# Optimization experiments

Measured on AMD Instinct MI355X. Metric: run time of the kernel, lower is better.

Reference implementation:

```python
import jax, jax.numpy as jnp
import numpy as np

N = 50000      # nodes
E = 800000     # edges (avg degree 16)
IN = 128       # input feature dim
D = 128        # embed dim (heads=1, concat)
SLOPE = 0.2    # GATv2Conv default negative_slope


def setup_inputs() -> dict:
    key = jax.random.key(0)
    ks = jax.random.split(key, 16)
    s_in = 1.0 / np.sqrt(IN)
    s_d = 1.0 / np.sqrt(D)
    inp = {
        "node_fts": jax.random.normal(ks[0], (N, IN), dtype=jnp.float32),
        "edge_index": jax.random.randint(ks[1], (2, E), 0, N, dtype=jnp.int64),
        # layer 1 (in_dim -> embed_dim)
        "Wl1": jax.random.normal(ks[2], (IN, D), dtype=jnp.float32) * s_in,
        "bl1": jnp.zeros((D,), dtype=jnp.float32),
        "Wr1": jax.random.normal(ks[3], (IN, D), dtype=jnp.float32) * s_in,
        "br1": jnp.zeros((D,), dtype=jnp.float32),
        "att1": jax.random.normal(ks[4], (D,), dtype=jnp.float32) * s_d,
        "bias1": jnp.zeros((D,), dtype=jnp.float32),
        # layer 2 (embed_dim -> embed_dim)
        "Wl2": jax.random.normal(ks[5], (D, D), dtype=jnp.float32) * s_d,
        "bl2": jnp.zeros((D,), dtype=jnp.float32),
        "Wr2": jax.random.normal(ks[6], (D, D), dtype=jnp.float32) * s_d,
        "br2": jnp.zeros((D,), dtype=jnp.float32),
        "att2": jax.random.normal(ks[7], (D,), dtype=jnp.float32) * s_d,
        "bias2": jnp.zeros((D,), dtype=jnp.float32),
    }
    return inp


def gatv2_layer(x, src, dst, Wl, bl, Wr, br, att, bias):
    # GATv2Conv (heads=1, share_weights=False):
    #   x_j (source message features) = lin_l(x), x_i (target) = lin_r(x)
    xl = x @ Wl + bl                                      # [N, D]
    xr = x @ Wr + br                                      # [N, D]
    e = jax.nn.leaky_relu(xl[src] + xr[dst], SLOPE)       # [E, D]
    logits = e @ att                                      # [E]
    # softmax over incoming edges of each target node
    m = jax.ops.segment_max(logits, dst, num_segments=N)  # [N], -inf for isolated
    m = jnp.where(jnp.isneginf(m), 0.0, m)
    a = jnp.exp(logits - m[dst])                          # [E]
    s = jax.ops.segment_sum(a, dst, num_segments=N)       # [N]
    a = a / jnp.maximum(s[dst], 1e-16)
    out = jax.ops.segment_sum(a[:, None] * xl[src], dst, num_segments=N)  # [N, D]
    return out + bias


def reference(node_fts, edge_index,
              Wl1, bl1, Wr1, br1, att1, bias1,
              Wl2, bl2, Wr2, br2, att2, bias2):
    src, dst = edge_index[0], edge_index[1]
    x = jax.nn.relu(gatv2_layer(node_fts, src, dst, Wl1, bl1, Wr1, br1, att1, bias1))
    x = jax.nn.relu(gatv2_layer(x, src, dst, Wl2, bl2, Wr2, br2, att2, bias2))
    return x
```

## Files before the change

kernel.cpp:

```cpp
#include <hip/hip_runtime.h>
#include <hip/hip_bf16.h>
#include <hip/hip_fp16.h>

#define N_NODES 50000
#define N_EDGES 800000
#define DIM 128
#define NGROUPS (N_NODES / 16)
#define LROW2 132
#define KBUCKET 196
#define BCAP 5120
#define EPB 2000

typedef __attribute__((ext_vector_type(8))) _Float16 hfrag8;
typedef __attribute__((ext_vector_type(4))) float f32x4;
typedef _Float16 h2 __attribute__((ext_vector_type(2)));

__device__ __forceinline__ h2 u2h(uint u){ union{uint u; h2 h;} c; c.u = u; return c.h; }


__global__ __launch_bounds__(256) void bucket_scatter_k(
    const int* __restrict__ src, const int* __restrict__ dst,
    int* __restrict__ bucket_cnt, uint* __restrict__ bucketdata)
{
  __shared__ int cnt[KBUCKET], base[KBUCKET], cur[KBUCKET];
  int tid = threadIdx.x;
  for (int t = tid; t < KBUCKET; t += 256) { cnt[t] = 0; cur[t] = 0; }
  __syncthreads();
  int e0 = blockIdx.x * EPB;
  int dreg[8];
  #pragma unroll
  for (int it = 0; it < 8; it++) {
    int i = it*256 + tid;
    dreg[it] = (i < EPB) ? dst[e0 + i] : -1;
    if (i < EPB) atomicAdd(&cnt[dreg[it] >> 8], 1);
  }
  __syncthreads();
  for (int t = tid; t < KBUCKET; t += 256)
    base[t] = atomicAdd(&bucket_cnt[t], cnt[t]);
  __syncthreads();
  #pragma unroll
  for (int it = 0; it < 8; it++) {
    int i = it*256 + tid;
    if (i < EPB) {
      int s = src[e0 + i], d = dreg[it];
      int b = d >> 8;
      int r = atomicAdd(&cur[b], 1);
      bucketdata[(size_t)b * BCAP + base[b] + r] = ((uint)s << 8) | (uint)(d & 255);
    }
  }
}

__global__ __launch_bounds__(64) void prep_w(
    const float* __restrict__ Wl1, const float* __restrict__ Wr1,
    const float* __restrict__ Wl2, const float* __restrict__ Wr2,
    _Float16* __restrict__ wb, int* __restrict__ bucket_cnt)
{
  int bid = blockIdx.x;
  if (bid == 0) {
    for (int t = threadIdx.x; t < KBUCKET; t += 64) bucket_cnt[t] = 0;
  }
  int layer = bid >> 6, rest = bid & 63;
  int C = rest >> 4, g = rest & 15;
  int lane = threadIdx.x;
  int m = lane & 15, q = lane >> 4;
  int dim = g*16 + m;
  const float* W = layer ? (dim < 128 ? Wl2 : Wr2) : (dim < 128 ? Wl1 : Wr1);
  int dcol = dim & 127;
  _Float16 h[8];
  #pragma unroll
  for (int j = 0; j < 8; j++) {
    int k = C*32 + q*8 + j;
    h[j] = (_Float16)W[(size_t)k*DIM + dcol];
  }
  size_t off = ((size_t)bid*64 + lane)*8;
  *(hfrag8*)(wb + off) = *(hfrag8*)h;
}

__global__ __launch_bounds__(256) void gemm1_csr_k(
    const float* __restrict__ x, const _Float16* __restrict__ wb,
    const float* __restrict__ bl, const float* __restrict__ br,
    __half* __restrict__ xlh, __half* __restrict__ xrh,
    const int* __restrict__ bucket_cnt, const uint* __restrict__ bucketdata,
    int* __restrict__ row_start, int* __restrict__ csr_src)
{
  __shared__ float lds[4][16*LROW2];
  __shared__ int hist[256], cur[256];
  __shared__ int wsumA[4], wsumB[4];
  int tid = threadIdx.x;

  if (blockIdx.x < KBUCKET) {
    int b = blockIdx.x;
    int lane = tid & 63, w = tid >> 6;
    int vv = (tid < b) ? bucket_cnt[tid] : 0;
    #pragma unroll
    for (int off = 32; off > 0; off >>= 1) vv += __shfl_xor(vv, off, 64);
    if (lane == 0) wsumA[w] = vv;
    hist[tid] = 0;
    __syncthreads();
    int base_csr = wsumA[0] + wsumA[1] + wsumA[2] + wsumA[3];
    int cnt = bucket_cnt[b];
    int node0 = b << 8;
    const uint* bd = bucketdata + (size_t)b * BCAP;
    for (int i = tid; i < cnt; i += 256)
      atomicAdd(&hist[bd[i] & 255], 1);
    __syncthreads();
    int v = hist[tid];
    int inc = v;
    #pragma unroll
    for (int off = 1; off < 64; off <<= 1) {
      int y = __shfl_up(inc, off, 64);
      if (lane >= off) inc += y;
    }
    if (lane == 63) wsumB[w] = inc;
    __syncthreads();
    int wpre = 0;
    #pragma unroll
    for (int i = 0; i < 4; i++) if (i < w) wpre += wsumB[i];
    int excl = wpre + inc - v;
    int node = node0 + tid;
    if (node < N_NODES) row_start[node] = base_csr + excl;
    if (b == 0 && tid == 0) row_start[N_NODES] = N_EDGES;
    cur[tid] = excl;
    __syncthreads();
    for (int i = tid; i < cnt; i += 256) {
      uint p = bd[i];
      int r = atomicAdd(&cur[p & 255], 1);
      csr_src[base_csr + r] = (int)(p >> 8);
    }
    return;
  }

  int wv = tid >> 6, lane = tid & 63;
  int G = (blockIdx.x - KBUCKET) * 4 + wv;
  if (G >= NGROUPS) return;

  int m = lane & 15, q = lane >> 4;
  const float* xrow = x + (size_t)(G*16 + m)*DIM + q*8;

  f32x4 acc[16];
  #pragma unroll
  for (int g = 0; g < 16; g++) acc[g] = (f32x4)(0.f);

  #pragma unroll 1
  for (int C = 0; C < 4; C++) {
    float v[8];
    *(float4*)(v)     = *(const float4*)(xrow + C*32);
    *(float4*)(v + 4) = *(const float4*)(xrow + C*32 + 4);
    _Float16 hh[8];
    #pragma unroll
    for (int j = 0; j < 8; j++) hh[j] = (_Float16)v[j];
    hfrag8 ah = *(hfrag8*)hh;
    #pragma unroll
    for (int g = 0; g < 16; g++) {
      size_t boff = ((size_t)(C*16 + g)*64 + lane)*8;
      hfrag8 bh = *(const hfrag8*)(wb + boff);
      acc[g] = __builtin_amdgcn_mfma_f32_16x16x32_f16(ah, bh, acc[g], 0, 0, 0);
    }
  }

  float* wlds = lds[wv];
  int dcol = (lane & 31) * 4;
  int rowsel = lane >> 5;
  #pragma unroll
  for (int half = 0; half < 2; half++) {
    #pragma unroll
    for (int g = 0; g < 8; g++) {
      #pragma unroll
      for (int r = 0; r < 4; r++)
        wlds[(q*4 + r)*LROW2 + g*16 + m] = acc[half*8 + g][r];
    }
    const float* B = half ? br : bl;
    ushort* outh = half ? (ushort*)xrh : (ushort*)xlh;
    float4 bv = *(const float4*)(B + dcol);
    #pragma unroll
    for (int it = 0; it < 8; it++) {
      int i = it*2 + rowsel;
      float4 vv = *(const float4*)(wlds + i*LROW2 + dcol);
      int node = G*16 + i;
      __half2 h0 = __floats2half2_rn(vv.x + bv.x, vv.y + bv.y);
      __half2 h1 = __floats2half2_rn(vv.z + bv.z, vv.w + bv.w);
      uint2 pk = make_uint2(*(uint*)&h0, *(uint*)&h1);
      *(uint2*)(outh + (size_t)node*DIM + dcol) = pk;
    }
  }
}

__device__ __forceinline__ void gather_core(
    int node, int hl,
    const __half* __restrict__ xlh, const __half* __restrict__ xrh,
    const int* __restrict__ row_start, const int* __restrict__ csr_src,
    const float* __restrict__ att, const float* __restrict__ bias,
    float4& o0, float4& o1)
{
  int r0 = row_start[node];
  int deg = row_start[node + 1] - r0;
  int last = r0 + deg - 1;

  uint4 rx = *(const uint4*)((const ushort*)xrh + (size_t)node*DIM + hl*8);
  h2 xr01 = u2h(rx.x), xr23 = u2h(rx.y), xr45 = u2h(rx.z), xr67 = u2h(rx.w);
  const float* ap = att + hl*8;
  float4 af0 = *(const float4*)(ap);
  float4 af1 = *(const float4*)(ap + 4);
  h2 a01 = {(_Float16)af0.x, (_Float16)af0.y};
  h2 a23 = {(_Float16)af0.z, (_Float16)af0.w};
  h2 a45 = {(_Float16)af1.x, (_Float16)af1.y};
  h2 a67 = {(_Float16)af1.z, (_Float16)af1.w};
  const h2 c02 = {(_Float16)0.2f, (_Float16)0.2f};

  float l = 0.f;
  float b0a=0,b1a=0,b2a=0,b3a=0,b4a=0,b5a=0,b6a=0,b7a=0;
  const ushort* xbase = (const ushort*)xlh + hl*8;

  for (int t = 0; t < deg; t += 8) {
    int idx[8];
    #pragma unroll
    for (int j = 0; j < 8; j++) {
      int rr = r0 + t + j;
      idx[j] = csr_src[rr <= last ? rr : last];
    }
    uint4 raw[8];
    #pragma unroll
    for (int j = 0; j < 8; j++)
      raw[j] = *(const uint4*)(xbase + (size_t)idx[j]*DIM);
    #pragma unroll
    for (int j = 0; j < 8; j++) {
      h2 v01 = u2h(raw[j].x), v23 = u2h(raw[j].y);
      h2 v45 = u2h(raw[j].z), v67 = u2h(raw[j].w);
      h2 s01 = v01 + xr01, s23 = v23 + xr23;
      h2 s45 = v45 + xr45, s67 = v67 + xr67;
      s01 = __builtin_elementwise_max(s01, s01 * c02);
      s23 = __builtin_elementwise_max(s23, s23 * c02);
      s45 = __builtin_elementwise_max(s45, s45 * c02);
      s67 = __builtin_elementwise_max(s67, s67 * c02);
      float p = __builtin_amdgcn_fdot2(s01, a01, 0.f, false);
      p = __builtin_amdgcn_fdot2(s23, a23, p, false);
      p = __builtin_amdgcn_fdot2(s45, a45, p, false);
      p = __builtin_amdgcn_fdot2(s67, a67, p, false);
      #pragma unroll
      for (int o = 1; o <= 8; o <<= 1) p += __shfl_xor(p, o, 64);
      float w = (t + j < deg) ? __expf(p) : 0.f;
      l += w;
      b0a = fmaf(w, (float)v01.x, b0a); b1a = fmaf(w, (float)v01.y, b1a);
      b2a = fmaf(w, (float)v23.x, b2a); b3a = fmaf(w, (float)v23.y, b3a);
      b4a = fmaf(w, (float)v45.x, b4a); b5a = fmaf(w, (float)v45.y, b5a);
      b6a = fmaf(w, (float)v67.x, b6a); b7a = fmaf(w, (float)v67.y, b7a);
    }
  }

  float inv = 1.f / fmaxf(l, 1e-16f);
  const float* bp = bias + hl*8;
  float4 c0 = *(const float4*)(bp);
  float4 c1 = *(const float4*)(bp + 4);
  o0.x = fmaxf(fmaf(b0a, inv, c0.x), 0.f);
  o0.y = fmaxf(fmaf(b1a, inv, c0.y), 0.f);
  o0.z = fmaxf(fmaf(b2a, inv, c0.z), 0.f);
  o0.w = fmaxf(fmaf(b3a, inv, c0.w), 0.f);
  o1.x = fmaxf(fmaf(b4a, inv, c1.x), 0.f);
  o1.y = fmaxf(fmaf(b5a, inv, c1.y), 0.f);
  o1.z = fmaxf(fmaf(b6a, inv, c1.z), 0.f);
  o1.w = fmaxf(fmaf(b7a, inv, c1.w), 0.f);
}

__global__ __launch_bounds__(256) void fused_g1_gemm2_k(
    const __half* __restrict__ xlh, const __half* __restrict__ xrh,
    const int* __restrict__ row_start, const int* __restrict__ csr_src,
    const float* __restrict__ att, const float* __restrict__ bias,
    const _Float16* __restrict__ wb2,
    const float* __restrict__ bl2, const float* __restrict__ br2,
    __half* __restrict__ xlh2, __half* __restrict__ xrh2)
{
  __shared__ ushort xs[16*128];
  __shared__ ushort outs[16*256];
  int tid = threadIdx.x;
  int wv = tid >> 6, lane = tid & 63;
  int q4 = lane >> 4, hl = lane & 15;
  int nl = wv*4 + q4;
  int base = blockIdx.x * 16;

  float4 o0, o1;
  gather_core(base + nl, hl, xlh, xrh, row_start, csr_src, att, bias, o0, o1);
  __half2 p0 = __floats2half2_rn(o0.x, o0.y);
  __half2 p1 = __floats2half2_rn(o0.z, o0.w);
  __half2 p2 = __floats2half2_rn(o1.x, o1.y);
  __half2 p3 = __floats2half2_rn(o1.z, o1.w);
  uint4 pk = make_uint4(*(uint*)&p0, *(uint*)&p1, *(uint*)&p2, *(uint*)&p3);
  *(uint4*)((char*)xs + nl*256 + ((hl*16) ^ ((nl&7)<<4))) = pk;
  __syncthreads();

  int m = lane & 15, q = lane >> 4;
  f32x4 acc[4];
  #pragma unroll
  for (int g = 0; g < 4; g++) acc[g] = (f32x4)(0.f);
  #pragma unroll
  for (int C = 0; C < 4; C++) {
    hfrag8 ah = *(const hfrag8*)((const char*)xs + m*256 + ((C*64 + q*16) ^ ((m&7)<<4)));
    #pragma unroll
    for (int g = 0; g < 4; g++) {
      int gg = wv*4 + g;
      size_t boff = ((size_t)(C*16 + gg)*64 + lane)*8;
      hfrag8 bh = *(const hfrag8*)(wb2 + boff);
      acc[g] = __builtin_amdgcn_mfma_f32_16x16x32_f16(ah, bh, acc[g], 0, 0, 0);
    }
  }
  #pragma unroll
  for (int g = 0; g < 4; g++) {
    int gg = wv*4 + g;
    int dim = gg*16 + m;
    float bv = (gg < 8) ? bl2[dim] : br2[dim - 128];
    #pragma unroll
    for (int r = 0; r < 4; r++) {
      int row = q*4 + r;
      __half hv = __float2half_rn(acc[g][r] + bv);
      outs[row*256 + gg*16 + m] = *(ushort*)&hv;
    }
  }
  __syncthreads();
  #pragma unroll
  for (int p = 0; p < 2; p++) {
    int c = p*256 + tid;
    int row = c >> 5, off = c & 31;
    uint4 v = *(const uint4*)((const char*)outs + row*512 + off*16);
    int nodeo = base + row;
    int d0 = off*8;
    ushort* dstp = (d0 < 128) ? ((ushort*)xlh2 + (size_t)nodeo*DIM + d0)
                              : ((ushort*)xrh2 + (size_t)nodeo*DIM + (d0 - 128));
    *(uint4*)dstp = v;
  }
}

__global__ __launch_bounds__(256) void gat_gather2(
    const __half* __restrict__ xlh, const __half* __restrict__ xrh,
    const int* __restrict__ row_start, const int* __restrict__ csr_src,
    const float* __restrict__ att, const float* __restrict__ bias,
    float* __restrict__ outf)
{
  int wave = (blockIdx.x * 256 + threadIdx.x) >> 6;
  int lane = threadIdx.x & 63;
  int q4 = lane >> 4;
  int hl = lane & 15;
  int node = wave * 4 + q4;
  float4 o0, o1;
  gather_core(node, hl, xlh, xrh, row_start, csr_src, att, bias, o0, o1);
  float* op = outf + (size_t)node*DIM + hl*8;
  *(float4*)(op)     = o0;
  *(float4*)(op + 4) = o1;
}

extern "C" void kernel_launch(void* const* d_in, const int* in_sizes, int n_in,
                              void* d_out, int out_size, void* d_ws, size_t ws_size,
                              hipStream_t stream)
{
  const float* node_fts = (const float*)d_in[0];
  const int*  edge_index = (const int*)d_in[1];
  const float* Wl1 = (const float*)d_in[2];
  const float* bl1 = (const float*)d_in[3];
  const float* Wr1 = (const float*)d_in[4];
  const float* br1 = (const float*)d_in[5];
  const float* att1 = (const float*)d_in[6];
  const float* bias1 = (const float*)d_in[7];
  const float* Wl2 = (const float*)d_in[8];
  const float* bl2 = (const float*)d_in[9];
  const float* Wr2 = (const float*)d_in[10];
  const float* br2 = (const float*)d_in[11];
  const float* att2 = (const float*)d_in[12];
  const float* bias2 = (const float*)d_in[13];
  const int* src = edge_index;
  const int* dst = edge_index + N_EDGES;

  char* ws = (char*)d_ws;
  __half* xlh = (__half*)ws;               ws += (size_t)N_NODES*DIM*2;
  __half* xrh = (__half*)ws;               ws += (size_t)N_NODES*DIM*2;
  __half* xlh2 = (__half*)ws;              ws += (size_t)N_NODES*DIM*2;
  __half* xrh2 = (__half*)ws;              ws += (size_t)N_NODES*DIM*2;
  _Float16* wb = (_Float16*)ws;            ws += 2*4*16*64*8*2;
  int* row_start   = (int*)ws;             ws += (N_NODES+1)*4;
  int* csr_src     = (int*)ws;             ws += (size_t)N_EDGES*4;
  int* bucket_cnt  = (int*)ws;             ws += KBUCKET*4;
  uint* bucketdata = (uint*)ws;            ws += (size_t)KBUCKET*BCAP*4;

  const int W_LAYER = 4*16*64*8;

  int gemm_blocks = (NGROUPS + 3) / 4;
  int gather_blocks = N_NODES / 16;

  prep_w<<<128, 64, 0, stream>>>(Wl1, Wr1, Wl2, Wr2, wb, bucket_cnt);
  bucket_scatter_k<<<N_EDGES/EPB, 256, 0, stream>>>(src, dst, bucket_cnt, bucketdata);
  gemm1_csr_k<<<KBUCKET + gemm_blocks, 256, 0, stream>>>(
      node_fts, wb, bl1, br1, xlh, xrh,
      bucket_cnt, bucketdata, row_start, csr_src);
  fused_g1_gemm2_k<<<NGROUPS, 256, 0, stream>>>(
      xlh, xrh, row_start, csr_src, att1, bias1,
      wb + W_LAYER, bl2, br2, xlh2, xrh2);
  gat_gather2<<<gather_blocks, 256, 0, stream>>>(
      xlh2, xrh2, row_start, csr_src, att2, bias2, (float*)d_out);
}
```

Baseline: 218.1 us.

## Degree-sort nodes per bucket, pipeline gather loads, use DPP reductions

Builds a per-bucket permutation that groups nodes by in-degree so waves processing four nodes have balanced loop trip counts, and runs both gather kernels over permuted slots. Stores pre-scaled byte offsets in the CSR to avoid index multiplies, double-buffers neighbor row loads in 4-edge halves to overlap memory with compute, and replaces shuffle-xor reductions with DPP row operations. Adds indirection through perm and padding slots, and the DPP shift-based reduction may not broadcast the sum to all lanes.

Result: slower. 229.9 us (+5.4%).

```diff
diff --git a/kernel.cpp b/kernel.cpp
--- a/kernel.cpp
+++ b/kernel.cpp
@@ -10,12 +10,23 @@
 #define KBUCKET 196
 #define BCAP 5120
 #define EPB 2000
+#define NSLOT (KBUCKET*256)
 
 typedef __attribute__((ext_vector_type(8))) _Float16 hfrag8;
 typedef __attribute__((ext_vector_type(4))) float f32x4;
 typedef _Float16 h2 __attribute__((ext_vector_type(2)));
 
 __device__ __forceinline__ h2 u2h(uint u){ union{uint u; h2 h;} c; c.u = u; return c.h; }
+
+__device__ __forceinline__ float rowsum16(float p) {
+  union { float f; int i; } a, b;
+  a.f = p;
+  b.i = __builtin_amdgcn_update_dpp(0, a.i, 0x128, 0xF, 0xF, true); a.f += b.f;
+  b.i = __builtin_amdgcn_update_dpp(0, a.i, 0x124, 0xF, 0xF, true); a.f += b.f;
+  b.i = __builtin_amdgcn_update_dpp(0, a.i, 0x122, 0xF, 0xF, true); a.f += b.f;
+  b.i = __builtin_amdgcn_update_dpp(0, a.i, 0x121, 0xF, 0xF, true); a.f += b.f;
+  return a.f;
+}
 
 
 __global__ __launch_bounds__(256) void bucket_scatter_k(
@@ -81,11 +92,13 @@
     const float* __restrict__ bl, const float* __restrict__ br,
     __half* __restrict__ xlh, __half* __restrict__ xrh,
     const int* __restrict__ bucket_cnt, const uint* __restrict__ bucketdata,
-    int* __restrict__ row_start, int* __restrict__ csr_src)
+    int* __restrict__ row_start, int* __restrict__ csr_soff,
+    int* __restrict__ perm)
 {
   __shared__ float lds[4][16*LROW2];
   __shared__ int hist[256], cur[256];
   __shared__ int wsumA[4], wsumB[4];
+  __shared__ int dhist[64], dbase[64], dcur[64];
   int tid = threadIdx.x;
 
   if (blockIdx.x < KBUCKET) {
@@ -96,6 +109,7 @@
     for (int off = 32; off > 0; off >>= 1) vv += __shfl_xor(vv, off, 64);
     if (lane == 0) wsumA[w] = vv;
     hist[tid] = 0;
+    if (tid < 64) { dhist[tid] = 0; dcur[tid] = 0; }
     __syncthreads();
     int base_csr = wsumA[0] + wsumA[1] + wsumA[2] + wsumA[3];
     int cnt = bucket_cnt[b];
@@ -105,6 +119,9 @@
       atomicAdd(&hist[bd[i] & 255], 1);
     __syncthreads();
     int v = hist[tid];
+    int node = node0 + tid;
+    int degc = (node < N_NODES) ? min(v, 63) : 63;
+    atomicAdd(&dhist[degc], 1);
     int inc = v;
     #pragma unroll
     for (int off = 1; off < 64; off <<= 1) {
@@ -117,15 +134,26 @@
     #pragma unroll
     for (int i = 0; i < 4; i++) if (i < w) wpre += wsumB[i];
     int excl = wpre + inc - v;
-    int node = node0 + tid;
     if (node < N_NODES) row_start[node] = base_csr + excl;
     if (b == 0 && tid == 0) row_start[N_NODES] = N_EDGES;
     cur[tid] = excl;
+    if (tid < 64) {
+      int c = dhist[tid];
+      int ic = c;
+      #pragma unroll
+      for (int off = 1; off < 64; off <<= 1) {
+        int y = __shfl_up(ic, off, 64);
+        if (tid >= off) ic += y;
+      }
+      dbase[tid] = ic - c;
+    }
     __syncthreads();
+    int rank = dbase[degc] + atomicAdd(&dcur[degc], 1);
+    perm[node0 + rank] = node;
     for (int i = tid; i < cnt; i += 256) {
       uint p = bd[i];
       int r = atomicAdd(&cur[p & 255], 1);
-      csr_src[base_csr + r] = (int)(p >> 8);
+      csr_soff[base_csr + r] = (int)(p & 0xFFFFFF00u);
     }
     return;
   }
@@ -175,25 +203,63 @@
     #pragma unroll
     for (int it = 0; it < 8; it++) {
       int i = it*2 + rowsel;
-      float4 vv = *(const float4*)(wlds + i*LROW2 + dcol);
+      float4 vv2 = *(const float4*)(wlds + i*LROW2 + dcol);
       int node = G*16 + i;
-      __half2 h0 = __floats2half2_rn(vv.x + bv.x, vv.y + bv.y);
-      __half2 h1 = __floats2half2_rn(vv.z + bv.z, vv.w + bv.w);
+      __half2 h0 = __floats2half2_rn(vv2.x + bv.x, vv2.y + bv.y);
+      __half2 h1 = __floats2half2_rn(vv2.z + bv.z, vv2.w + bv.w);
       uint2 pk = make_uint2(*(uint*)&h0, *(uint*)&h1);
       *(uint2*)(outh + (size_t)node*DIM + dcol) = pk;
     }
   }
 }
 
+
+#define GAT_LDI(OFF, TBASE)                                             \
+  _Pragma("unroll")                                                     \
+  for (int j = 0; j < 4; j++) {                                         \
+    int rr = r0 + (TBASE) + j;                                          \
+    OFF[j] = csr_soff[rr <= last ? rr : last];                          \
+  }
+
+#define GAT_LDR(OFF, RAW)                                               \
+  _Pragma("unroll")                                                     \
+  for (int j = 0; j < 4; j++)                                           \
+    RAW[j] = *(const uint4*)(xb + (size_t)(uint)OFF[j]);
+
+#define GAT_COMP(RAW, TBASE)                                            \
+  _Pragma("unroll")                                                     \
+  for (int j = 0; j < 4; j++) {                                         \
+    h2 v01 = u2h(RAW[j].x), v23 = u2h(RAW[j].y);                        \
+    h2 v45 = u2h(RAW[j].z), v67 = u2h(RAW[j].w);                        \
+    h2 s01 = v01 + xr01, s23 = v23 + xr23;                              \
+    h2 s45 = v45 + xr45, s67 = v67 + xr67;                              \
+    s01 = __builtin_elementwise_max(s01, s01 * c02);                    \
+    s23 = __builtin_elementwise_max(s23, s23 * c02);                    \
+    s45 = __builtin_elementwise_max(s45, s45 * c02);                    \
+    s67 = __builtin_elementwise_max(s67, s67 * c02);                    \
+    float pA = __builtin_amdgcn_fdot2(s01, a01, 0.f, false);            \
+    pA = __builtin_amdgcn_fdot2(s23, a23, pA, false);                   \
+    float pB = __builtin_amdgcn_fdot2(s45, a45, 0.f, false);            \
+    pB = __builtin_amdgcn_fdot2(s67, a67, pB, false);                   \
+    float p = rowsum16(pA + pB);                                        \
+    float w = ((TBASE) + j < deg) ? __expf(p) : 0.f;                    \
+    l += w;                                                             \
+    b0a = fmaf(w, (float)v01.x, b0a); b1a = fmaf(w, (float)v01.y, b1a); \
+    b2a = fmaf(w, (float)v23.x, b2a); b3a = fmaf(w, (float)v23.y, b3a); \
+    b4a = fmaf(w, (float)v45.x, b4a); b5a = fmaf(w, (float)v45.y, b5a); \
+    b6a = fmaf(w, (float)v67.x, b6a); b7a = fmaf(w, (float)v67.y, b7a); \
+  }
+
 __device__ __forceinline__ void gather_core(
-    int node, int hl,
+    int node, int valid, int hl,
     const __half* __restrict__ xlh, const __half* __restrict__ xrh,
-    const int* __restrict__ row_start, const int* __restrict__ csr_src,
+    const int* __restrict__ row_start, const int* __restrict__ csr_soff,
     const float* __restrict__ att, const float* __restrict__ bias,
     float4& o0, float4& o1)
 {
   int r0 = row_start[node];
   int deg = row_start[node + 1] - r0;
+  if (!valid) deg = 0;
   int last = r0 + deg - 1;
 
   uint4 rx = *(const uint4*)((const ushort*)xrh + (size_t)node*DIM + hl*8);
@@ -209,42 +275,18 @@
 
   float l = 0.f;
   float b0a=0,b1a=0,b2a=0,b3a=0,b4a=0,b5a=0,b6a=0,b7a=0;
-  const ushort* xbase = (const ushort*)xlh + hl*8;
-
+  const char* xb = (const char*)xlh + hl*16;
+
+  int offA[4]; uint4 rawA[4];
+  int offB[4]; uint4 rawB[4];
+
+  if (deg > 0) { GAT_LDI(offA, 0); GAT_LDR(offA, rawA); }
   for (int t = 0; t < deg; t += 8) {
-    int idx[8];
-    #pragma unroll
-    for (int j = 0; j < 8; j++) {
-      int rr = r0 + t + j;
-      idx[j] = csr_src[rr <= last ? rr : last];
-    }
-    uint4 raw[8];
-    #pragma unroll
-    for (int j = 0; j < 8; j++)
-      raw[j] = *(const uint4*)(xbase + (size_t)idx[j]*DIM);
-    #pragma unroll
-    for (int j = 0; j < 8; j++) {
-      h2 v01 = u2h(raw[j].x), v23 = u2h(raw[j].y);
-      h2 v45 = u2h(raw[j].z), v67 = u2h(raw[j].w);
-      h2 s01 = v01 + xr01, s23 = v23 + xr23;
-      h2 s45 = v45 + xr45, s67 = v67 + xr67;
-      s01 = __builtin_elementwise_max(s01, s01 * c02);
-      s23 = __builtin_elementwise_max(s23, s23 * c02);
-      s45 = __builtin_elementwise_max(s45, s45 * c02);
-      s67 = __builtin_elementwise_max(s67, s67 * c02);
-      float p = __builtin_amdgcn_fdot2(s01, a01, 0.f, false);
-      p = __builtin_amdgcn_fdot2(s23, a23, p, false);
-      p = __builtin_amdgcn_fdot2(s45, a45, p, false);
-      p = __builtin_amdgcn_fdot2(s67, a67, p, false);
-      #pragma unroll
-      for (int o = 1; o <= 8; o <<= 1) p += __shfl_xor(p, o, 64);
-      float w = (t + j < deg) ? __expf(p) : 0.f;
-      l += w;
-      b0a = fmaf(w, (float)v01.x, b0a); b1a = fmaf(w, (float)v01.y, b1a);
-      b2a = fmaf(w, (float)v23.x, b2a); b3a = fmaf(w, (float)v23.y, b3a);
-      b4a = fmaf(w, (float)v45.x, b4a); b5a = fmaf(w, (float)v45.y, b5a);
-      b6a = fmaf(w, (float)v67.x, b6a); b7a = fmaf(w, (float)v67.y, b7a);
-    }
+    bool hasB = (t + 4 < deg);
+    if (hasB) { GAT_LDI(offB, t + 4); GAT_LDR(offB, rawB); }
+    GAT_COMP(rawA, t);
+    if (t + 8 < deg) { GAT_LDI(offA, t + 8); GAT_LDR(offA, rawA); }
+    if (hasB) GAT_COMP(rawB, t + 4);
   }
 
   float inv = 1.f / fmaxf(l, 1e-16f);
@@ -263,7 +305,8 @@
 
 __global__ __launch_bounds__(256) void fused_g1_gemm2_k(
     const __half* __restrict__ xlh, const __half* __restrict__ xrh,
-    const int* __restrict__ row_start, const int* __restrict__ csr_src,
+    const int* __restrict__ row_start, const int* __restrict__ csr_soff,
+    const int* __restrict__ perm,
     const float* __restrict__ att, const float* __restrict__ bias,
     const _Float16* __restrict__ wb2,
     const float* __restrict__ bl2, const float* __restrict__ br2,
@@ -271,14 +314,19 @@
 {
   __shared__ ushort xs[16*128];
   __shared__ ushort outs[16*256];
+  __shared__ int nodes_s[16];
   int tid = threadIdx.x;
   int wv = tid >> 6, lane = tid & 63;
   int q4 = lane >> 4, hl = lane & 15;
   int nl = wv*4 + q4;
   int base = blockIdx.x * 16;
 
+  int node = perm[base + nl];
+  int valid = node < N_NODES;
+  int nodec = valid ? node : 0;
+  if (hl == 0) nodes_s[nl] = node;
   float4 o0, o1;
-  gather_core(base + nl, hl, xlh, xrh, row_start, csr_src, att, bias, o0, o1);
+  gather_core(nodec, valid, hl, xlh, xrh, row_start, csr_soff, att, bias, o0, o1);
   __half2 p0 = __floats2half2_rn(o0.x, o0.y);
   __half2 p1 = __floats2half2_rn(o0.z, o0.w);
   __half2 p2 = __floats2half2_rn(o1.x, o1.y);
@@ -320,7 +368,7 @@
     int c = p*256 + tid;
     int row = c >> 5, off = c & 31;
     uint4 v = *(const uint4*)((const char*)outs + row*512 + off*16);
-    int nodeo = base + row;
+    int nodeo = nodes_s[row];
     int d0 = off*8;
     ushort* dstp = (d0 < 128) ? ((ushort*)xlh2 + (size_t)nodeo*DIM + d0)
                               : ((ushort*)xrh2 + (size_t)nodeo*DIM + (d0 - 128));
@@ -330,7 +378,8 @@
 
 __global__ __launch_bounds__(256) void gat_gather2(
     const __half* __restrict__ xlh, const __half* __restrict__ xrh,
-    const int* __restrict__ row_start, const int* __restrict__ csr_src,
+    const int* __restrict__ row_start, const int* __restrict__ csr_soff,
+    const int* __restrict__ perm,
     const float* __restrict__ att, const float* __restrict__ bias,
     float* __restrict__ outf)
 {
@@ -338,12 +387,17 @@
   int lane = threadIdx.x & 63;
   int q4 = lane >> 4;
   int hl = lane & 15;
-  int node = wave * 4 + q4;
+  int slot = wave * 4 + q4;
+  int node = perm[slot];
+  int valid = node < N_NODES;
+  int nodec = valid ? node : 0;
   float4 o0, o1;
-  gather_core(node, hl, xlh, xrh, row_start, csr_src, att, bias, o0, o1);
-  float* op = outf + (size_t)node*DIM + hl*8;
-  *(float4*)(op)     = o0;
-  *(float4*)(op + 4) = o1;
+  gather_core(nodec, valid, hl, xlh, xrh, row_start, csr_soff, att, bias, o0, o1);
+  if (valid) {
+    float* op = outf + (size_t)node*DIM + hl*8;
+    *(float4*)(op)     = o0;
+    *(float4*)(op + 4) = o1;
+  }
 }
 
 extern "C" void kernel_launch(void* const* d_in, const int* in_sizes, int n_in,
@@ -370,27 +424,28 @@
   char* ws = (char*)d_ws;
   __half* xlh = (__half*)ws;               ws += (size_t)N_NODES*DIM*2;
   __half* xrh = (__half*)ws;               ws += (size_t)N_NODES*DIM*2;
-  __half* xlh2 = (__half*)ws;              ws += (size_t)N_NODES*DIM*2;
-  __half* xrh2 = (__half*)ws;              ws += (size_t)N_NODES*DIM*2;
+  __half* xlh2 = (__half*)ws;              ws += (size_t)NSLOT*DIM*2;
+  __half* xrh2 = (__half*)ws;              ws += (size_t)NSLOT*DIM*2;
   _Float16* wb = (_Float16*)ws;            ws += 2*4*16*64*8*2;
   int* row_start   = (int*)ws;             ws += (N_NODES+1)*4;
-  int* csr_src     = (int*)ws;             ws += (size_t)N_EDGES*4;
+  int* csr_soff    = (int*)ws;             ws += (size_t)N_EDGES*4;
+  int* perm        = (int*)ws;             ws += (size_t)NSLOT*4;
   int* bucket_cnt  = (int*)ws;             ws += KBUCKET*4;
   uint* bucketdata = (uint*)ws;            ws += (size_t)KBUCKET*BCAP*4;
 
   const int W_LAYER = 4*16*64*8;
 
   int gemm_blocks = (NGROUPS + 3) / 4;
-  int gather_blocks = N_NODES / 16;
+  int slot_blocks = NSLOT / 16;
 
   prep_w<<<128, 64, 0, stream>>>(Wl1, Wr1, Wl2, Wr2, wb, bucket_cnt);
   bucket_scatter_k<<<N_EDGES/EPB, 256, 0, stream>>>(src, dst, bucket_cnt, bucketdata);
   gemm1_csr_k<<<KBUCKET + gemm_blocks, 256, 0, stream>>>(
       node_fts, wb, bl1, br1, xlh, xrh,
-      bucket_cnt, bucketdata, row_start, csr_src);
-  fused_g1_gemm2_k<<<NGROUPS, 256, 0, stream>>>(
-      xlh, xrh, row_start, csr_src, att1, bias1,
+      bucket_cnt, bucketdata, row_start, csr_soff, perm);
+  fused_g1_gemm2_k<<<slot_blocks, 256, 0, stream>>>(
+      xlh, xrh, row_start, csr_soff, perm, att1, bias1,
       wb + W_LAYER, bl2, br2, xlh2, xrh2);
-  gat_gather2<<<gather_blocks, 256, 0, stream>>>(
-      xlh2, xrh2, row_start, csr_src, att2, bias2, (float*)d_out);
-}
+  gat_gather2<<<slot_blocks, 256, 0, stream>>>(
+      xlh2, xrh2, row_start, csr_soff, perm, att2, bias2, (float*)d_out);
+}
```
